# Optimization experiments

Measured on AMD Instinct MI355X. Metric: run time of the kernel, lower is better.

Reference implementation:

```python
import jax, jax.numpy as jnp
import numpy as np

D_MODEL = 1024
NUM_HEADS = 16
D_HEAD = D_MODEL // NUM_HEADS


def setup_inputs() -> dict:
    key = jax.random.key(0)
    k1, k2, k3, k4, k5 = jax.random.split(key, 5)
    s = 1.0 / np.sqrt(D_MODEL)
    return {
        "x": jax.random.normal(k1, (4, 2048, D_MODEL), dtype=jnp.float32),
        "W_qkv": jax.random.normal(k2, (D_MODEL, 3 * D_MODEL), dtype=jnp.float32) * s,
        "b_qkv": jnp.zeros((3 * D_MODEL,), dtype=jnp.float32),
        "W_out": jax.random.normal(k3, (D_MODEL, D_MODEL), dtype=jnp.float32) * s,
        "b_out": jnp.zeros((D_MODEL,), dtype=jnp.float32),
    }


def reference(x, W_qkv, b_qkv, W_out, b_out):
    B, T, D = x.shape
    qkv = x @ W_qkv + b_qkv  # [B,T,3D]
    q, k, v = jnp.split(qkv, 3, axis=-1)
    # [B,T,D] -> [B,H,T,dh]
    def to_heads(t):
        return t.reshape(B, T, NUM_HEADS, D_HEAD).transpose(0, 2, 1, 3)
    q, k, v = to_heads(q), to_heads(k), to_heads(v)
    scores = jnp.einsum("bhqd,bhkd->bhqk", q, k) / jnp.sqrt(jnp.float32(D_HEAD))
    attn = jax.nn.softmax(scores, axis=-1)
    out = jnp.einsum("bhqk,bhkd->bhqd", attn, v)
    out = out.transpose(0, 2, 1, 3).reshape(B, T, D)
    return out @ W_out + b_out
```

## Files before the change

kernel.cpp:

```cpp
#include <hip/hip_runtime.h>

typedef unsigned short u16;
typedef unsigned int u32;
typedef u16 u16x4 __attribute__((ext_vector_type(4)));
typedef u16 u16x8 __attribute__((ext_vector_type(8)));
typedef u32 u32x2 __attribute__((ext_vector_type(2)));
typedef u32 u32x4 __attribute__((ext_vector_type(4)));
typedef __bf16 bf16x2 __attribute__((ext_vector_type(2)));
typedef __bf16 bf16x8 __attribute__((ext_vector_type(8)));
typedef float f32x4 __attribute__((ext_vector_type(4)));

__device__ __forceinline__ u16 f2bf(float f) {
  return __builtin_bit_cast(u16, (__bf16)f);
}

__device__ __forceinline__ u32 packbf2(float lo, float hi) {
  bf16x2 t;
  t[0] = (__bf16)lo;
  t[1] = (__bf16)hi;
  return __builtin_bit_cast(u32, t);
}

__device__ __forceinline__ f32x4 mfma16(bf16x8 a, bf16x8 b, f32x4 c) {
  return __builtin_amdgcn_mfma_f32_16x16x32_bf16(a, b, c, 0, 0, 0);
}

#define GLOAD_LDS16(gsrc, ldst)                                              \
  __builtin_amdgcn_global_load_lds(                                          \
      (const __attribute__((address_space(1))) void*)(gsrc),                 \
      (__attribute__((address_space(3))) void*)(ldst), 16, 0, 0)

__global__ __launch_bounds__(256) void cvt_x(const float* __restrict__ in,
                                             u16* __restrict__ out, int n) {
  int i = (blockIdx.x * 256 + threadIdx.x) * 8;
  if (i >= n) return;
  u16x8 o;
#pragma unroll
  for (int j = 0; j < 8; j++) o[j] = f2bf(in[i + j]);
  *(u16x8*)&out[i] = o;
}

__global__ __launch_bounds__(256) void transpose_cvt(const float* __restrict__ in,
                                                     u16* __restrict__ out,
                                                     int R, int C) {
  __shared__ float tile[32][33];
  int gx = blockIdx.x * 32, gy = blockIdx.y * 32;
  int tx = threadIdx.x, ty = threadIdx.y;
#pragma unroll
  for (int i = 0; i < 4; i++)
    tile[ty + i * 8][tx] = in[(size_t)(gy + ty + i * 8) * C + gx + tx];
  __syncthreads();
#pragma unroll
  for (int i = 0; i < 4; i++) {
    int c = ty + i * 8;
    out[(size_t)(gx + c) * R + gy + tx] = f2bf(tile[tx][c]);
  }
}

template <int EPI, int GX>
__global__ __launch_bounds__(256, 3) void gemm_bf16(
    const u16* __restrict__ A, const u16* __restrict__ Bt,
    const float* __restrict__ bias, u16* __restrict__ qb, u16* __restrict__ kb,
    u16* __restrict__ vb, float* __restrict__ fout, int N, int K) {
  __shared__ u16 As[3][128 * 32];
  __shared__ u16 Bs[3][128 * 32];
  const int tid = threadIdx.x;
  const int wave = tid >> 6;
  const int lane = tid & 63;
  const int wr = wave >> 1, wc = wave & 1;
  const int l15 = lane & 15, l4 = lane >> 4;

  const int id = blockIdx.y * GX + blockIdx.x;
  const int xcd = id & 7;
  const int j = id >> 3;
  const int bm = (xcd * 8 + j / GX) * 128;
  const int bn = (j % GX) * 128;

  const int srow = wave * 16 + (lane >> 2);
  const int slch = lane & 3;
  const int ldst = wave * 512;

  const u16* Abase = A + (size_t)bm * K;
  const u16* Bbase = Bt + (size_t)bn * K;

  f32x4 acc[4][4] = {};

  auto STAGE = [&](int buf, int k0) {
#pragma unroll
    for (int c = 0; c < 2; c++) {
      const int row = c * 64 + srow;
      const int sch = slch ^ ((row >> 1) & 3);
      GLOAD_LDS16(Abase + (size_t)row * K + k0 + sch * 8,
                  &As[buf][c * 2048 + ldst]);
      GLOAD_LDS16(Bbase + (size_t)row * K + k0 + sch * 8,
                  &Bs[buf][c * 2048 + ldst]);
    }
  };

  const int NT = K >> 5;
  STAGE(0, 0);
  STAGE(1, 32);
  int cur = 0;
  for (int t = 0; t < NT; ++t) {
    if (t + 1 < NT) {
      asm volatile("s_waitcnt lgkmcnt(0)\n\ts_waitcnt vmcnt(4)" ::: "memory");
    } else {
      asm volatile("s_waitcnt lgkmcnt(0)\n\ts_waitcnt vmcnt(0)" ::: "memory");
    }
    __builtin_amdgcn_sched_barrier(0);
    asm volatile("s_barrier" ::: "memory");

    if (t + 2 < NT) {
      int stg = cur + 2;
      if (stg >= 3) stg -= 3;
      STAGE(stg, (t + 2) * 32);
    }

    const u16* as = As[cur];
    const u16* bs = Bs[cur];
    bf16x8 af[4], bfr[4];
#pragma unroll
    for (int mi = 0; mi < 4; mi++) {
      const int row = wr * 64 + mi * 16 + l15;
      af[mi] = *(const bf16x8*)&as[row * 32 + ((l4 ^ ((row >> 1) & 3)) * 8)];
    }
#pragma unroll
    for (int ni = 0; ni < 4; ni++) {
      const int row = wc * 64 + ni * 16 + l15;
      bfr[ni] = *(const bf16x8*)&bs[row * 32 + ((l4 ^ ((row >> 1) & 3)) * 8)];
    }
    __builtin_amdgcn_s_setprio(1);
#pragma unroll
    for (int mi = 0; mi < 4; mi++)
#pragma unroll
      for (int ni = 0; ni < 4; ni++)
        acc[mi][ni] = mfma16(af[mi], bfr[ni], acc[mi][ni]);
    __builtin_amdgcn_s_setprio(0);
    cur = (cur == 2) ? 0 : cur + 1;
  }

#pragma unroll
  for (int mi = 0; mi < 4; mi++) {
#pragma unroll
    for (int ni = 0; ni < 4; ni++) {
      const int col = bn + wc * 64 + ni * 16 + l15;
      const float bv = bias[col];
      const int row0 = bm + wr * 64 + mi * 16 + l4 * 4;
      if (EPI == 0) {
        const int which = col >> 10;
        const int hc = col & 1023;
        const int h = hc >> 6, d = hc & 63;
#pragma unroll
        for (int r = 0; r < 4; r++) {
          const int row = row0 + r;
          const int b = row >> 11, t = row & 2047;
          const float v = acc[mi][ni][r] + bv;
          if (which == 0)
            qb[((size_t)(b * 16 + h) * 2048 + t) * 64 + d] = f2bf(v * 0.18033688f);
          else if (which == 1)
            kb[((size_t)(b * 16 + h) * 2048 + t) * 64 + d] = f2bf(v);
          else {
            const int o = t & 63;
            const int op = (o & 3) | (((o >> 4) & 1) << 2) | (((o >> 2) & 3) << 3) |
                           ((o >> 5) << 5);
            const int tp = (t & ~63) | op;
            vb[((size_t)(b * 16 + h) * 64 + d) * 2048 + tp] = f2bf(v);
          }
        }
      } else {
#pragma unroll
        for (int r = 0; r < 4; r++)
          fout[(size_t)(row0 + r) * N + col] = acc[mi][ni][r] + bv;
      }
    }
  }
}

__global__ __launch_bounds__(256, 4) void attn_kernel(const u16* __restrict__ Q,
                                                      const u16* __restrict__ Kg,
                                                      const u16* __restrict__ Vt,
                                                      u16* __restrict__ O) {
  __shared__ u16 Ks[2][64 * 64];
  __shared__ u16 Vs[2][64 * 64];
  const int tid = threadIdx.x;
  const int wave = tid >> 6;
  const int lane = tid & 63;
  const int l15 = lane & 15, l4 = lane >> 4;

  const int id = blockIdx.y * 16 + blockIdx.x;
  const int xcd = id & 7;
  const int j = id >> 3;
  const int bh = xcd * 8 + (j >> 4);
  const int qt = j & 15;

  const u16* qg = Q + ((size_t)bh * 2048 + qt * 128 + wave * 32) * 64;
  bf16x8 qf[2][2];
#pragma unroll
  for (int mi = 0; mi < 2; mi++)
#pragma unroll
    for (int kg2 = 0; kg2 < 2; kg2++)
      qf[mi][kg2] = *(const bf16x8*)&qg[(mi * 16 + l15) * 64 + kg2 * 32 + l4 * 8];

  float mrow[2] = {-1e30f, -1e30f};
  float lrow[2] = {0.f, 0.f};
  f32x4 oacc[4][2] = {};

  const int srow = wave * 8 + (lane >> 3);
  const int slch = lane & 7;
  const int ldst = wave * 512;
  const u16* kbase = Kg + (size_t)bh * 2048 * 64;
  const u16* vbase = Vt + (size_t)bh * 64 * 2048;

  auto STAGE = [&](int buf, int kt) {
#pragma unroll
    for (int c = 0; c < 2; c++) {
      const int row = c * 32 + srow;
      const int sch = slch ^ (row & 7);
      GLOAD_LDS16(kbase + (size_t)(kt * 64 + row) * 64 + sch * 8,
                  &Ks[buf][c * 2048 + ldst]);
      GLOAD_LDS16(vbase + (size_t)row * 2048 + kt * 64 + sch * 8,
                  &Vs[buf][c * 2048 + ldst]);
    }
  };

  STAGE(0, 0);
  int cur = 0;
  for (int kt = 0; kt < 32; kt++) {
    __syncthreads();
    if (kt + 1 < 32) STAGE(cur ^ 1, kt + 1);
    const u16* ks = Ks[cur];
    const u16* vs = Vs[cur];

    f32x4 sacc[2][4] = {};
    __builtin_amdgcn_s_setprio(1);
#pragma unroll
    for (int kg2 = 0; kg2 < 2; kg2++) {
#pragma unroll
      for (int ni = 0; ni < 4; ni++) {
        const int row = ni * 16 + l15;
        bf16x8 kf =
            *(const bf16x8*)&ks[row * 64 + (((kg2 * 4 + l4) ^ (row & 7)) * 8)];
#pragma unroll
        for (int mi = 0; mi < 2; mi++)
          sacc[mi][ni] = mfma16(kf, qf[mi][kg2], sacc[mi][ni]);
      }
    }
    __builtin_amdgcn_s_setprio(0);

#pragma unroll
    for (int mi = 0; mi < 2; mi++) {
      float pm0 = fmaxf(fmaxf(sacc[mi][0][0], sacc[mi][0][1]),
                        fmaxf(sacc[mi][0][2], sacc[mi][0][3]));
      float pm1 = fmaxf(fmaxf(sacc[mi][1][0], sacc[mi][1][1]),
                        fmaxf(sacc[mi][1][2], sacc[mi][1][3]));
      float pm2 = fmaxf(fmaxf(sacc[mi][2][0], sacc[mi][2][1]),
                        fmaxf(sacc[mi][2][2], sacc[mi][2][3]));
      float pm3 = fmaxf(fmaxf(sacc[mi][3][0], sacc[mi][3][1]),
                        fmaxf(sacc[mi][3][2], sacc[mi][3][3]));
      float pm = fmaxf(fmaxf(pm0, pm1), fmaxf(pm2, pm3));
      pm = fmaxf(pm, __shfl_xor(pm, 16));
      pm = fmaxf(pm, __shfl_xor(pm, 32));
      const bool noskip = !__all(pm - mrow[mi] <= 6.0f);
      float mnew = mrow[mi];
      if (noskip) {
        mnew = fmaxf(mrow[mi], pm);
        const float alpha = __builtin_amdgcn_exp2f(mrow[mi] - mnew);
        mrow[mi] = mnew;
        lrow[mi] *= alpha;
#pragma unroll
        for (int di = 0; di < 4; di++) oacc[di][mi] *= alpha;
      }
      float rs = 0.f;
#pragma unroll
      for (int ni = 0; ni < 4; ni++)
#pragma unroll
        for (int r = 0; r < 4; r++) {
          const float p = __builtin_amdgcn_exp2f(sacc[mi][ni][r] - mnew);
          sacc[mi][ni][r] = p;
          rs += p;
        }
      rs += __shfl_xor(rs, 16);
      rs += __shfl_xor(rs, 32);
      lrow[mi] += rs;
    }

#pragma unroll
    for (int kg2 = 0; kg2 < 2; kg2++) {
      bf16x8 pf[2];
#pragma unroll
      for (int mi = 0; mi < 2; mi++) {
        u32x4 praw;
        praw[0] = packbf2(sacc[mi][2 * kg2][0], sacc[mi][2 * kg2][1]);
        praw[1] = packbf2(sacc[mi][2 * kg2][2], sacc[mi][2 * kg2][3]);
        praw[2] = packbf2(sacc[mi][2 * kg2 + 1][0], sacc[mi][2 * kg2 + 1][1]);
        praw[3] = packbf2(sacc[mi][2 * kg2 + 1][2], sacc[mi][2 * kg2 + 1][3]);
        pf[mi] = __builtin_bit_cast(bf16x8, praw);
      }
      __builtin_amdgcn_s_setprio(1);
#pragma unroll
      for (int di = 0; di < 4; di++) {
        const int row = di * 16 + l15;
        bf16x8 vf =
            *(const bf16x8*)&vs[row * 64 + (((kg2 * 4 + l4) ^ (row & 7)) * 8)];
#pragma unroll
        for (int mi = 0; mi < 2; mi++)
          oacc[di][mi] = mfma16(vf, pf[mi], oacc[di][mi]);
      }
      __builtin_amdgcn_s_setprio(0);
    }
    cur ^= 1;
  }

  const int b = bh >> 4, h = bh & 15;
#pragma unroll
  for (int mi = 0; mi < 2; mi++) {
    const float invl = 1.0f / lrow[mi];
    const int t = qt * 128 + wave * 32 + mi * 16 + l15;
#pragma unroll
    for (int di = 0; di < 4; di++) {
      u16x4 o;
#pragma unroll
      for (int r = 0; r < 4; r++) o[r] = f2bf(oacc[di][mi][r] * invl);
      *(u16x4*)&O[((size_t)b * 2048 + t) * 1024 + h * 64 + di * 16 + l4 * 4] = o;
    }
  }
}

extern "C" void kernel_launch(void* const* d_in, const int* in_sizes, int n_in,
                              void* d_out, int out_size, void* d_ws, size_t ws_size,
                              hipStream_t stream) {
  const float* x = (const float*)d_in[0];
  const float* Wqkv = (const float*)d_in[1];
  const float* bqkv = (const float*)d_in[2];
  const float* Wout = (const float*)d_in[3];
  const float* bout = (const float*)d_in[4];
  float* out = (float*)d_out;

  u16* ws = (u16*)d_ws;
  u16* xb = ws;
  u16* wqT = xb + 8388608;
  u16* woT = wqT + 3145728;
  u16* qb = woT + 1048576;
  u16* kb = qb + 8388608;
  u16* vb = kb + 8388608;
  u16* ao = vb + 8388608;

  cvt_x<<<4096, 256, 0, stream>>>(x, xb, 8388608);
  transpose_cvt<<<dim3(96, 32), dim3(32, 8), 0, stream>>>(Wqkv, wqT, 1024, 3072);
  transpose_cvt<<<dim3(32, 32), dim3(32, 8), 0, stream>>>(Wout, woT, 1024, 1024);
  gemm_bf16<0, 24><<<dim3(24, 64), 256, 0, stream>>>(xb, wqT, bqkv, qb, kb, vb,
                                                     nullptr, 3072, 1024);
  attn_kernel<<<dim3(16, 64), 256, 0, stream>>>(qb, kb, vb, ao);
  gemm_bf16<1, 8><<<dim3(8, 64), 256, 0, stream>>>(ao, woT, bout, nullptr,
                                                   nullptr, nullptr, out, 1024, 1024);
}
```

Before: 216.4 us.

## Use 256x256 tiles with 8 waves for the QKV projection GEMM

```diff
diff --git a/kernel.cpp b/kernel.cpp
--- a/kernel.cpp
+++ b/kernel.cpp
@@ -57,45 +57,45 @@
   }
 }
 
-template <int EPI, int GX>
-__global__ __launch_bounds__(256, 3) void gemm_bf16(
+__global__ __launch_bounds__(512, 1) void gemm256(
     const u16* __restrict__ A, const u16* __restrict__ Bt,
     const float* __restrict__ bias, u16* __restrict__ qb, u16* __restrict__ kb,
-    u16* __restrict__ vb, float* __restrict__ fout, int N, int K) {
-  __shared__ u16 As[3][128 * 32];
-  __shared__ u16 Bs[3][128 * 32];
+    u16* __restrict__ vb, int N, int K, int NBN) {
+  extern __shared__ u16 lds[];
   const int tid = threadIdx.x;
-  const int wave = tid >> 6;
+  const int wid = tid >> 6;
   const int lane = tid & 63;
-  const int wr = wave >> 1, wc = wave & 1;
+  const int wr = wid >> 2, wc = wid & 3;
   const int l15 = lane & 15, l4 = lane >> 4;
 
-  const int id = blockIdx.y * GX + blockIdx.x;
-  const int xcd = id & 7;
-  const int j = id >> 3;
-  const int bm = (xcd * 8 + j / GX) * 128;
-  const int bn = (j % GX) * 128;
-
-  const int srow = wave * 16 + (lane >> 2);
-  const int slch = lane & 3;
-  const int ldst = wave * 512;
-
-  const u16* Abase = A + (size_t)bm * K;
-  const u16* Bbase = Bt + (size_t)bn * K;
-
-  f32x4 acc[4][4] = {};
-
-  auto STAGE = [&](int buf, int k0) {
+  const int nb = gridDim.x;
+  const int id2 = (blockIdx.x & 7) * (nb >> 3) + (blockIdx.x >> 3);
+  const int bm = (id2 / NBN) * 256;
+  const int bn = (id2 % NBN) * 256;
+
+  const u16* Ab = A + (size_t)bm * K;
+  const u16* Bb = Bt + (size_t)bn * K;
+
+#define ABUF(b) (lds + (b) * 8192)
+#define BBUF(b) (lds + 24576 + (b) * 8192)
+
+  const int srow = tid >> 2;
+  const int slch = tid & 3;
+  const int ldst = wid * 512;
+
+  auto STAGE = [&](int b, int k0) {
 #pragma unroll
     for (int c = 0; c < 2; c++) {
-      const int row = c * 64 + srow;
+      const int row = c * 128 + srow;
       const int sch = slch ^ ((row >> 1) & 3);
-      GLOAD_LDS16(Abase + (size_t)row * K + k0 + sch * 8,
-                  &As[buf][c * 2048 + ldst]);
-      GLOAD_LDS16(Bbase + (size_t)row * K + k0 + sch * 8,
-                  &Bs[buf][c * 2048 + ldst]);
+      GLOAD_LDS16(Ab + (size_t)row * K + k0 + sch * 8,
+                  ABUF(b) + c * 4096 + ldst);
+      GLOAD_LDS16(Bb + (size_t)row * K + k0 + sch * 8,
+                  BBUF(b) + c * 4096 + ldst);
     }
   };
+
+  f32x4 acc[8][4] = {};
 
   const int NT = K >> 5;
   STAGE(0, 0);
@@ -116,12 +116,12 @@
       STAGE(stg, (t + 2) * 32);
     }
 
-    const u16* as = As[cur];
-    const u16* bs = Bs[cur];
-    bf16x8 af[4], bfr[4];
-#pragma unroll
-    for (int mi = 0; mi < 4; mi++) {
-      const int row = wr * 64 + mi * 16 + l15;
+    const u16* as = ABUF(cur);
+    const u16* bs = BBUF(cur);
+    bf16x8 af[8], bfr[4];
+#pragma unroll
+    for (int mi = 0; mi < 8; mi++) {
+      const int row = wr * 128 + mi * 16 + l15;
       af[mi] = *(const bf16x8*)&as[row * 32 + ((l4 ^ ((row >> 1) & 3)) * 8)];
     }
 #pragma unroll
@@ -131,7 +131,7 @@
     }
     __builtin_amdgcn_s_setprio(1);
 #pragma unroll
-    for (int mi = 0; mi < 4; mi++)
+    for (int mi = 0; mi < 8; mi++)
 #pragma unroll
       for (int ni = 0; ni < 4; ni++)
         acc[mi][ni] = mfma16(af[mi], bfr[ni], acc[mi][ni]);
@@ -140,38 +140,129 @@
   }
 
 #pragma unroll
+  for (int mi = 0; mi < 8; mi++) {
+#pragma unroll
+    for (int ni = 0; ni < 4; ni++) {
+      const int col = bn + wc * 64 + ni * 16 + l15;
+      const float bv = bias[col];
+      const int row0 = bm + wr * 128 + mi * 16 + l4 * 4;
+      const int which = col >> 10;
+      const int hc = col & 1023;
+      const int h = hc >> 6, d = hc & 63;
+#pragma unroll
+      for (int r = 0; r < 4; r++) {
+        const int row = row0 + r;
+        const int b = row >> 11, tt = row & 2047;
+        const float v = acc[mi][ni][r] + bv;
+        if (which == 0)
+          qb[((size_t)(b * 16 + h) * 2048 + tt) * 64 + d] = f2bf(v * 0.18033688f);
+        else if (which == 1)
+          kb[((size_t)(b * 16 + h) * 2048 + tt) * 64 + d] = f2bf(v);
+        else {
+          const int o = tt & 63;
+          const int op = (o & 3) | (((o >> 4) & 1) << 2) |
+                         (((o >> 2) & 3) << 3) | ((o >> 5) << 5);
+          const int tp = (tt & ~63) | op;
+          vb[((size_t)(b * 16 + h) * 64 + d) * 2048 + tp] = f2bf(v);
+        }
+      }
+    }
+  }
+#undef ABUF
+#undef BBUF
+}
+
+template <int GX>
+__global__ __launch_bounds__(256, 3) void gemm_proj(
+    const u16* __restrict__ A, const u16* __restrict__ Bt,
+    const float* __restrict__ bias, float* __restrict__ fout, int N, int K) {
+  __shared__ u16 As[3][128 * 32];
+  __shared__ u16 Bs[3][128 * 32];
+  const int tid = threadIdx.x;
+  const int wave = tid >> 6;
+  const int lane = tid & 63;
+  const int wr = wave >> 1, wc = wave & 1;
+  const int l15 = lane & 15, l4 = lane >> 4;
+
+  const int id = blockIdx.y * GX + blockIdx.x;
+  const int xcd = id & 7;
+  const int j = id >> 3;
+  const int bm = (xcd * 8 + j / GX) * 128;
+  const int bn = (j % GX) * 128;
+
+  const int srow = wave * 16 + (lane >> 2);
+  const int slch = lane & 3;
+  const int ldst = wave * 512;
+
+  const u16* Abase = A + (size_t)bm * K;
+  const u16* Bbase = Bt + (size_t)bn * K;
+
+  f32x4 acc[4][4] = {};
+
+  auto STAGE = [&](int buf, int k0) {
+#pragma unroll
+    for (int c = 0; c < 2; c++) {
+      const int row = c * 64 + srow;
+      const int sch = slch ^ ((row >> 1) & 3);
+      GLOAD_LDS16(Abase + (size_t)row * K + k0 + sch * 8,
+                  &As[buf][c * 2048 + ldst]);
+      GLOAD_LDS16(Bbase + (size_t)row * K + k0 + sch * 8,
+                  &Bs[buf][c * 2048 + ldst]);
+    }
+  };
+
+  const int NT = K >> 5;
+  STAGE(0, 0);
+  STAGE(1, 32);
+  int cur = 0;
+  for (int t = 0; t < NT; ++t) {
+    if (t + 1 < NT) {
+      asm volatile("s_waitcnt lgkmcnt(0)\n\ts_waitcnt vmcnt(4)" ::: "memory");
+    } else {
+      asm volatile("s_waitcnt lgkmcnt(0)\n\ts_waitcnt vmcnt(0)" ::: "memory");
+    }
+    __builtin_amdgcn_sched_barrier(0);
+    asm volatile("s_barrier" ::: "memory");
+
+    if (t + 2 < NT) {
+      int stg = cur + 2;
+      if (stg >= 3) stg -= 3;
+      STAGE(stg, (t + 2) * 32);
+    }
+
+    const u16* as = As[cur];
+    const u16* bs = Bs[cur];
+    bf16x8 af[4], bfr[4];
+#pragma unroll
+    for (int mi = 0; mi < 4; mi++) {
+      const int row = wr * 64 + mi * 16 + l15;
+      af[mi] = *(const bf16x8*)&as[row * 32 + ((l4 ^ ((row >> 1) & 3)) * 8)];
+    }
+#pragma unroll
+    for (int ni = 0; ni < 4; ni++) {
+      const int row = wc * 64 + ni * 16 + l15;
+      bfr[ni] = *(const bf16x8*)&bs[row * 32 + ((l4 ^ ((row >> 1) & 3)) * 8)];
+    }
+    __builtin_amdgcn_s_setprio(1);
+#pragma unroll
+    for (int mi = 0; mi < 4; mi++)
+#pragma unroll
+      for (int ni = 0; ni < 4; ni++)
+        acc[mi][ni] = mfma16(af[mi], bfr[ni], acc[mi][ni]);
+    __builtin_amdgcn_s_setprio(0);
+    cur = (cur == 2) ? 0 : cur + 1;
+  }
+
+#pragma unroll
   for (int mi = 0; mi < 4; mi++) {
 #pragma unroll
     for (int ni = 0; ni < 4; ni++) {
       const int col = bn + wc * 64 + ni * 16 + l15;
       const float bv = bias[col];
       const int row0 = bm + wr * 64 + mi * 16 + l4 * 4;
-      if (EPI == 0) {
-        const int which = col >> 10;
-        const int hc = col & 1023;
-        const int h = hc >> 6, d = hc & 63;
-#pragma unroll
-        for (int r = 0; r < 4; r++) {
-          const int row = row0 + r;
-          const int b = row >> 11, t = row & 2047;
-          const float v = acc[mi][ni][r] + bv;
-          if (which == 0)
-            qb[((size_t)(b * 16 + h) * 2048 + t) * 64 + d] = f2bf(v * 0.18033688f);
-          else if (which == 1)
-            kb[((size_t)(b * 16 + h) * 2048 + t) * 64 + d] = f2bf(v);
-          else {
-            const int o = t & 63;
-            const int op = (o & 3) | (((o >> 4) & 1) << 2) | (((o >> 2) & 3) << 3) |
-                           ((o >> 5) << 5);
-            const int tp = (t & ~63) | op;
-            vb[((size_t)(b * 16 + h) * 64 + d) * 2048 + tp] = f2bf(v);
-          }
-        }
-      } else {
-#pragma unroll
-        for (int r = 0; r < 4; r++)
-          fout[(size_t)(row0 + r) * N + col] = acc[mi][ni][r] + bv;
-      }
+#pragma unroll
+      for (int r = 0; r < 4; r++)
+        fout[(size_t)(row0 + r) * N + col] = acc[mi][ni][r] + bv;
     }
   }
 }
@@ -345,12 +436,13 @@
   u16* vb = kb + 8388608;
   u16* ao = vb + 8388608;
 
+  hipFuncSetAttribute((const void*)gemm256,
+                      hipFuncAttributeMaxDynamicSharedMemorySize, 98304);
+
   cvt_x<<<4096, 256, 0, stream>>>(x, xb, 8388608);
   transpose_cvt<<<dim3(96, 32), dim3(32, 8), 0, stream>>>(Wqkv, wqT, 1024, 3072);
   transpose_cvt<<<dim3(32, 32), dim3(32, 8), 0, stream>>>(Wout, woT, 1024, 1024);
-  gemm_bf16<0, 24><<<dim3(24, 64), 256, 0, stream>>>(xb, wqT, bqkv, qb, kb, vb,
-                                                     nullptr, 3072, 1024);
+  gemm256<<<384, 512, 98304, stream>>>(xb, wqT, bqkv, qb, kb, vb, 3072, 1024, 12);
   attn_kernel<<<dim3(16, 64), 256, 0, stream>>>(qb, kb, vb, ao);
-  gemm_bf16<1, 8><<<dim3(8, 64), 256, 0, stream>>>(ao, woT, bout, nullptr,
-                                                   nullptr, nullptr, out, 1024, 1024);
-}
+  gemm_proj<8><<<dim3(8, 64), 256, 0, stream>>>(ao, woT, bout, out, 1024, 1024);
+}
```

Result: slower. 229.2 us (+5.9%).
